# Kernel tuning notes

Measured on AMD Instinct MI355X. Metric: run time of the kernel, lower is better.

## Reference

```python
import jax, jax.numpy as jnp
import numpy as np

B, NC, NT = 1, 128, 256
F = 8                       # fidnet filters (both 1h and 13c)
KH, KW = 5, 8               # fidnet kernel
DILS = [1, 2, 3, 4, 6, 8, 10, 12, 14, 16, 18, 20, 24, 28, 32]
BLOCKS = 3
L = BLOCKS * len(DILS)      # 45 wave layers per FIDNetLayer
RSTEPS, RK = 4, 9           # refine steps / refine kernel


def dfh_tanh(x):
    return jnp.tanh(x) * 0.98 + x * 0.02


def dfh_sigmoid(x):
    return jax.nn.sigmoid(x) * 0.98 + x * 0.02


def dfh_relu(x):
    return jax.nn.relu(x) * 0.98 + x * 0.02


def conv2d(x, w, b, dil_w=1, padding='VALID'):
    # x: NHWC, w: HWIO
    out = jax.lax.conv_general_dilated(x, w, (1, 1), padding,
                                       rhs_dilation=(1, dil_w),
                                       dimension_numbers=('NHWC', 'HWIO', 'NHWC'))
    return out + b


def hilbert(x):
    # analytic signal along last axis (real input, even length)
    N = x.shape[-1]
    hh = jnp.concatenate([jnp.ones(1, jnp.float32), 2.0 * jnp.ones(N // 2 - 1, jnp.float32),
                          jnp.ones(1, jnp.float32), jnp.zeros(N // 2 - 1, jnp.float32)]).astype(jnp.complex64)
    return jnp.fft.ifft(jnp.fft.fft(x.astype(jnp.complex64)) * hh)


def fidnet_layer(x, dw, db, wy1, by1, wy2, by2, wz0, bz0):
    # WaveNet-style stack of gated dilated convs with residuals + skip sum
    x = dfh_tanh(x @ dw + db)            # (B,H,W,2F)
    skip = jnp.zeros_like(x)
    ph = (KH - 1) // 2
    for i in range(wy1.shape[0]):
        dil = DILS[i % len(DILS)]
        xin = jnp.pad(x, ((0, 0), (ph, ph), (0, dil * (KW - 1)), (0, 0)))
        y1 = dfh_tanh(conv2d(xin, wy1[i], by1[i], dil))
        y2 = dfh_sigmoid(conv2d(xin, wy2[i], by2[i], dil))
        z = jnp.pad(y1 * y2, ((0, 0), (ph, ph), (0, KW - 1), (0, 0)))
        z = conv2d(z, wz0[i], bz0[i], 1)
        skip = skip + z
        x = z + x
    return dfh_tanh(skip)


def setup_inputs():
    key = jax.random.key(0)
    ks = jax.random.split(key, 16)
    n = lambda k, s, sc=0.05: jax.random.normal(k, s, jnp.float32) * sc
    return {
        'times': n(ks[0], (B, 2, NT), 1.0),
        'times_in': n(ks[1], (B, NC), 1.0),
        'inp_2d_nc': n(ks[2], (B, 1, NC, NT), 1.0),
        'inp_2d_c': n(ks[3], (B, 1, NC, NT), 1.0),
        'c_dense_w': n(ks[4], (4, 2 * F)), 'c_dense_b': jnp.zeros((2 * F,), jnp.float32),
        'c_wy1': n(ks[5], (L, KH, KW, 2 * F, F)), 'c_by1': jnp.zeros((L, F), jnp.float32),
        'c_wy2': n(ks[6], (L, KH, KW, 2 * F, F)), 'c_by2': jnp.zeros((L, F), jnp.float32),
        'c_wz0': n(ks[7], (L, KH, KW, F, 2 * F)), 'c_bz0': jnp.zeros((L, 2 * F), jnp.float32),
        'h_dense_w': n(ks[8], (2 * F, 2 * F)), 'h_dense_b': jnp.zeros((2 * F,), jnp.float32),
        'h_wy1': n(ks[9], (L, KH, KW, 2 * F, F)), 'h_by1': jnp.zeros((L, F), jnp.float32),
        'h_wy2': n(ks[10], (L, KH, KW, 2 * F, F)), 'h_by2': jnp.zeros((L, F), jnp.float32),
        'h_wz0': n(ks[11], (L, KH, KW, F, 2 * F)), 'h_bz0': jnp.zeros((L, 2 * F), jnp.float32),
        'ref_wr': n(ks[12], (RSTEPS, RK, RK, 8 * F, 4 * F), 0.02), 'ref_br': jnp.zeros((RSTEPS, 4 * F), jnp.float32),
        'ref_wt': n(ks[13], (RSTEPS, RK, RK, 8 * F, 4 * F), 0.02), 'ref_bt': jnp.zeros((RSTEPS, 4 * F), jnp.float32),
        'dense_w': n(ks[14], (12 * F, 2)), 'dense_b': jnp.zeros((2,), jnp.float32),
    }


def reference(times, times_in, inp_2d_nc, inp_2d_c,
              c_dense_w, c_dense_b, c_wy1, c_by1, c_wy2, c_by2, c_wz0, c_bz0,
              h_dense_w, h_dense_b, h_wy1, h_by1, h_wy2, h_by2, h_wz0, h_bz0,
              ref_wr, ref_br, ref_wt, ref_bt, dense_w, dense_b):
    Bn, _, nc, nt = inp_2d_nc.shape
    # build 4-channel input plane (B, NT, NC, 4)
    times_plane = jnp.tile(times[:, :1, :], (1, nc, 1))[:, None]          # (B,1,NC,NT)
    times_in_plane = jnp.tile(times_in[:, :, None], (1, 1, nt))[:, None]  # (B,1,NC,NT)
    tr = lambda a: jnp.transpose(a, (0, 3, 2, 1))
    inp = jnp.concatenate([tr(inp_2d_nc), tr(inp_2d_c), tr(times_plane), tr(times_in_plane)], axis=-1)

    cout = fidnet_layer(inp, c_dense_w, c_dense_b, c_wy1, c_by1, c_wy2, c_by2, c_wz0, c_bz0)  # (B,NT,NC,2F)
    cout = jnp.transpose(cout, (0, 3, 1, 2))               # (B,2F,NT,NC)
    cout = jnp.pad(cout, ((0, 0), (0, 0), (0, 0), (0, nc)))  # (B,2F,NT,2NC)
    mult = jnp.concatenate([jnp.full((1,), 0.5, jnp.float32), jnp.ones(nc - 1, jnp.float32)])
    multc = mult.astype(jnp.complex64)
    cout_ft = jnp.fft.fftshift(jnp.fft.fft(multc * (cout[..., 0::2] + 1j * cout[..., 1::2])), axes=-1)
    cout_ft = jnp.transpose(jnp.real(cout_ft), (0, 1, 3, 2))  # (B,2F,NC,NT)
    cout_ft = hilbert(cout_ft)
    hinp = jnp.conj(jnp.fft.fft(jnp.fft.fftshift(cout_ft, axes=-1)) / nt)
    mult_pad = jnp.pad(mult, (0, nt - nc), constant_values=1.0).astype(jnp.complex64)
    hinp = hinp / mult_pad
    zero_mask = jnp.where(jnp.abs(times[:, 0, 2::2]) > 0.0, 1.0, 0.0)
    zero_mask = jnp.pad(zero_mask, ((0, 0), (1, 0)), constant_values=1.0)[:, None, None, :]  # (B,1,1,NT//2)
    hinp = hinp[..., :nt // 2] * zero_mask
    hinp = jnp.stack([jnp.real(hinp), jnp.imag(hinp)], axis=-1).reshape(Bn, 2 * F, nc, nt)
    hinp = jnp.transpose(hinp, (0, 2, 3, 1)).astype(jnp.float32)  # (B,NC,NT,2F)

    hout = fidnet_layer(hinp, h_dense_w, h_dense_b, h_wy1, h_by1, h_wy2, h_by2, h_wz0, h_bz0)
    hout = jnp.concatenate([hout, hinp], axis=-1)          # (B,NC,NT,4F)
    hout = jnp.transpose(hout, (0, 3, 1, 2))               # (B,4F,NC,NT)
    hout = jnp.pad(hout, ((0, 0), (0, 0), (0, 0), (0, nt)))
    winH = jnp.concatenate([jnp.full((1,), 0.5, jnp.float32), jnp.ones(nt - 1, jnp.float32)]).astype(jnp.complex64)
    hout_ft = jnp.fft.fftshift(jnp.fft.fft(winH * (hout[..., 0::2] + 1j * hout[..., 1::2])), axes=-1)
    hout_ft = jnp.transpose(jnp.real(hout_ft), (0, 2, 3, 1))  # (B,NC,NT,4F)

    fnorm = jnp.max(jnp.abs(hout_ft), axis=(1, 2, 3), keepdims=True)
    ref = jnp.tile(hout_ft / fnorm, (1, 1, 1, 2))          # (B,NC,NT,8F)
    for i in range(ref_wr.shape[0]):
        rr = dfh_relu(conv2d(ref, ref_wr[i], ref_br[i], 1, 'SAME'))
        tt = dfh_tanh(conv2d(ref, ref_wt[i], ref_bt[i], 1, 'SAME'))
        ref = jnp.concatenate([tt, rr], axis=-1) + ref
    ref = ref * fnorm
    hfin = jnp.concatenate([ref, hout_ft], axis=-1) @ dense_w + dense_b  # (B,NC,NT,2)
    return jnp.stack([hfin[..., 0], hfin[..., 1] / fnorm[..., 0]], axis=-1)
```

## Files before the change

### kernel.cpp

```cpp
#include <hip/hip_runtime.h>

#define NTT 256
#define NCC 128

typedef __attribute__((ext_vector_type(8))) short bf16x8;
typedef __attribute__((ext_vector_type(4))) float f32x4;

__device__ __forceinline__ float dfh_tanh_f(float v){ return tanhf(v)*0.98f + 0.02f*v; }
__device__ __forceinline__ float dfh_sig_f(float v){ return 0.98f/(1.f+expf(-v)) + 0.02f*v; }
__device__ __forceinline__ unsigned f2bf(float x){
  unsigned u = __float_as_uint(x);
  return (u + 0x7fffu + ((u>>16)&1u)) >> 16;
}

__global__ __launch_bounds__(256) void k_build_c(
    const float* __restrict__ times, const float* __restrict__ times_in,
    const float* __restrict__ i2nc, const float* __restrict__ i2c,
    const float* __restrict__ dw, const float* __restrict__ db,
    float* __restrict__ x, unsigned short* __restrict__ xb,
    float* __restrict__ skip)
{
  int gid = blockIdx.x*256 + threadIdx.x;
  if (gid >= NTT*NCC) return;
  int c = gid & 127, t = gid >> 7;
  float v0 = i2nc[c*NTT + t];
  float v1 = i2c [c*NTT + t];
  float v2 = times[t];
  float v3 = times_in[c];
  #pragma unroll
  for (int f=0; f<16; ++f){
    float a = v0*dw[f] + v1*dw[16+f] + v2*dw[32+f] + v3*dw[48+f] + db[f];
    float xv = dfh_tanh_f(a);
    x[gid*16+f]    = xv;
    xb[gid*16+f]   = (unsigned short)f2bf(xv);
    skip[gid*16+f] = 0.f;
  }
}

__global__ __launch_bounds__(256) void k_build_h(
    const float* __restrict__ hinp, const float* __restrict__ dw,
    const float* __restrict__ db, float* __restrict__ x,
    unsigned short* __restrict__ xb, float* __restrict__ skip)
{
  int gid = blockIdx.x*256 + threadIdx.x;
  if (gid >= NCC*NTT) return;
  const float* in = hinp + gid*16;
  float iv[16];
  #pragma unroll
  for (int i=0;i<16;i++) iv[i]=in[i];
  #pragma unroll
  for (int f=0; f<16; ++f){
    float a = db[f];
    #pragma unroll
    for (int i=0;i<16;i++) a += iv[i]*dw[i*16+f];
    float xv = dfh_tanh_f(a);
    x[gid*16+f]    = xv;
    xb[gid*16+f]   = (unsigned short)f2bf(xv);
    skip[gid*16+f] = 0.f;
  }
}

__global__ __launch_bounds__(256) void k_wpack(
    const float* __restrict__ cwy1, const float* __restrict__ cwy2,
    const float* __restrict__ cwz0,
    const float* __restrict__ hwy1, const float* __restrict__ hwy2,
    const float* __restrict__ hwz0,
    unsigned short* __restrict__ gfrag, unsigned short* __restrict__ zfrag)
{
  int tid = blockIdx.x*256 + threadIdx.x;
  if (tid < 115200){
    int lane = tid & 63, ks = (tid>>6) % 20, layer = tid / 1280;
    const float* w1 = (layer < 45) ? cwy1 + layer*5120 : hwy1 + (layer-45)*5120;
    const float* w2 = (layer < 45) ? cwy2 + layer*5120 : hwy2 + (layer-45)*5120;
    int n = lane & 15;
    unsigned pk[4];
    #pragma unroll
    for (int jj=0; jj<4; ++jj){
      unsigned hl[2];
      #pragma unroll
      for (int h2=0; h2<2; ++h2){
        int k = ks*32 + (lane>>4)*8 + jj*2 + h2;
        int tap = k>>4, ci = k&15;
        float v = (n<8) ? w1[(tap*16+ci)*8 + n] : w2[(tap*16+ci)*8 + (n-8)];
        hl[h2] = f2bf(v);
      }
      pk[jj] = hl[0] | (hl[1]<<16);
    }
    uint4 v4; v4.x=pk[0]; v4.y=pk[1]; v4.z=pk[2]; v4.w=pk[3];
    *reinterpret_cast<uint4*>(gfrag + (size_t)tid*8) = v4;
  } else if (tid < 172800){
    int t2 = tid - 115200;
    int lane = t2 & 63, ks = (t2>>6) % 10, layer = t2 / 640;
    const float* wz = (layer < 45) ? cwz0 + layer*5120 : hwz0 + (layer-45)*5120;
    int n = lane & 15;
    unsigned pk[4];
    #pragma unroll
    for (int jj=0; jj<4; ++jj){
      unsigned hl[2];
      #pragma unroll
      for (int h2=0; h2<2; ++h2){
        int k = ks*32 + (lane>>4)*8 + jj*2 + h2;
        int tap = k>>3, ci = k&7;
        hl[h2] = f2bf(wz[(tap*8+ci)*16 + n]);
      }
      pk[jj] = hl[0] | (hl[1]<<16);
    }
    uint4 v4; v4.x=pk[0]; v4.y=pk[1]; v4.z=pk[2]; v4.w=pk[3];
    *reinterpret_cast<uint4*>(zfrag + (size_t)t2*8) = v4;
  }
}

template<int W>
__global__ __launch_bounds__(512) void k_gate_mfma(
    const unsigned short* __restrict__ xb, unsigned short* __restrict__ gb,
    const unsigned short* __restrict__ bfrag,
    const float* __restrict__ by1, const float* __restrict__ by2,
    int H, int dil)
{
  __shared__ __align__(16) unsigned short lds[(10*W+1)*8];
  const int tid = threadIdx.x, lane = tid & 63, wv = tid >> 6;
  const int nb = W/128;
  const int bid = blockIdx.x;
  const int wg = (bid & 7) * (gridDim.x >> 3) + (bid >> 3);
  const int h  = wg / nb;
  const int w0 = (wg % nb) * 128;
  const int NE = 10*W;

  bf16x8 bfr[20];
  #pragma unroll
  for (int ks = 0; ks < 20; ++ks)
    bfr[ks] = *reinterpret_cast<const bf16x8*>(bfrag + (ks*64 + lane)*8);

  for (int q = tid; q < NE; q += 512){
    int q2 = q >> 1, chunk = q & 1;
    int col = q2 % W, r = q2 / W;
    int hh = h + r - 2;
    uint4 v = make_uint4(0u,0u,0u,0u);
    if (hh >= 0 && hh < H)
      v = *reinterpret_cast<const uint4*>(xb + ((size_t)(hh*W+col))*16 + chunk*8);
    *reinterpret_cast<uint4*>(lds + ((r*2+chunk)*W + col)*8) = v;
  }
  if (tid == 0) *reinterpret_cast<uint4*>(lds + (size_t)NE*8) = make_uint4(0u,0u,0u,0u);
  __syncthreads();

  f32x4 acc0 = (f32x4){0.f,0.f,0.f,0.f};
  f32x4 acc1 = (f32x4){0.f,0.f,0.f,0.f};
  const int wbase = w0 + wv*16;
  const int zoff = NE*8;
  #pragma unroll
  for (int ks = 0; ks < 20; ++ks){
    int kh = ks >> 2, kw0 = (ks & 3)*2;
    if (w0 + dil*kw0 >= W) continue;
    int kw = kw0 + (lane>>5);
    int chunk = (lane>>4) & 1;
    int col = wbase + (lane&15) + dil*kw;
    int off = (col < W) ? ((kh*2+chunk)*W + col)*8 : zoff;
    bf16x8 a = *reinterpret_cast<const bf16x8*>(lds + off);
    if (ks & 1) acc1 = __builtin_amdgcn_mfma_f32_16x16x32_bf16(a, bfr[ks], acc1, 0,0,0);
    else        acc0 = __builtin_amdgcn_mfma_f32_16x16x32_bf16(a, bfr[ks], acc0, 0,0,0);
  }

  int n = lane & 15;
  float b1 = by1[n & 7], b2 = by2[n & 7];
  #pragma unroll
  for (int ri=0; ri<4; ++ri){
    float av = acc0[ri] + acc1[ri];
    float own = av + b1;
    float oth = __shfl_xor(av, 8) + b2;
    if (n < 8){
      float gv = dfh_tanh_f(own) * dfh_sig_f(oth);
      int w = wbase + (lane>>4)*4 + ri;
      gb[((size_t)(h*W + w))*8 + n] = (unsigned short)f2bf(gv);
    }
  }
}

template<int W>
__global__ __launch_bounds__(512) void k_zres_mfma(
    const unsigned short* __restrict__ gb,
    float* __restrict__ x, unsigned short* __restrict__ xb,
    float* __restrict__ skip,
    const unsigned short* __restrict__ bfrag,
    const float* __restrict__ bz, int H)
{
  __shared__ __align__(16) unsigned short lds[(5*W+1)*8];
  const int tid = threadIdx.x, lane = tid & 63, wv = tid >> 6;
  const int nb = W/128;
  const int bid = blockIdx.x;
  const int wg = (bid & 7) * (gridDim.x >> 3) + (bid >> 3);
  const int h  = wg / nb;
  const int w0 = (wg % nb) * 128;

  bf16x8 bfr[10];
  #pragma unroll
  for (int ks = 0; ks < 10; ++ks)
    bfr[ks] = *reinterpret_cast<const bf16x8*>(bfrag + (ks*64 + lane)*8);

  for (int q = tid; q < 5*W; q += 512){
    int col = q % W, r = q / W;
    int hh = h + r - 2;
    uint4 v = make_uint4(0u,0u,0u,0u);
    if (hh >= 0 && hh < H)
      v = *reinterpret_cast<const uint4*>(gb + ((size_t)(hh*W+col))*8);
    *reinterpret_cast<uint4*>(lds + (r*W+col)*8) = v;
  }
  if (tid == 0) *reinterpret_cast<uint4*>(lds + (size_t)(5*W)*8) = make_uint4(0u,0u,0u,0u);
  __syncthreads();

  f32x4 acc0 = (f32x4){0.f,0.f,0.f,0.f};
  f32x4 acc1 = (f32x4){0.f,0.f,0.f,0.f};
  const int wbase = w0 + wv*16;
  const int zoff = 5*W*8;
  #pragma unroll
  for (int ks = 0; ks < 10; ++ks){
    int kh = ks >> 1, kw = (ks & 1)*4 + (lane>>4);
    int col = wbase + (lane&15) + kw;
    int off = (col < W) ? (kh*W + col)*8 : zoff;
    bf16x8 a = *reinterpret_cast<const bf16x8*>(lds + off);
    if (ks & 1) acc1 = __builtin_amdgcn_mfma_f32_16x16x32_bf16(a, bfr[ks], acc1, 0,0,0);
    else        acc0 = __builtin_amdgcn_mfma_f32_16x16x32_bf16(a, bfr[ks], acc0, 0,0,0);
  }

  int n = lane & 15;
  float bv = bz[n];
  #pragma unroll
  for (int ri=0; ri<4; ++ri){
    int w = wbase + (lane>>4)*4 + ri;
    size_t idx = ((size_t)(h*W + w))*16 + n;
    float z = acc0[ri] + acc1[ri] + bv;
    skip[idx] += z;
    float xn = x[idx] + z;
    x[idx]  = xn;
    xb[idx] = (unsigned short)f2bf(xn);
  }
}

__global__ __launch_bounds__(256) void k_dtanh_t(const float* __restrict__ s,
                                                 float* __restrict__ o)
{
  __shared__ float tile[256][17];
  int c = blockIdx.x;
  int tid = threadIdx.x;
  int f = tid & 15, tq = tid >> 4;
  #pragma unroll
  for (int p = 0; p < 16; ++p){
    int t = p*16 + tq;
    tile[t][f] = s[((size_t)t*128 + c)*16 + f];
  }
  __syncthreads();
  int t = tid;
  #pragma unroll
  for (int f2 = 0; f2 < 16; ++f2)
    o[(size_t)f2*32768 + c*256 + t] = dfh_tanh_f(tile[t][f2]);
}

__global__ __launch_bounds__(256) void k_dft_c1(const float* __restrict__ cout,
                                                float* __restrict__ cft)
{
  __shared__ float ctab[128], stab[128];
  int tid = threadIdx.x;
  if (tid < 128){
    float ang = (float)tid * (6.283185307179586f/128.f);
    ctab[tid] = cosf(ang); stab[tid] = sinf(ang);
  }
  __syncthreads();
  int gid = blockIdx.x*256 + tid;
  int t = gid & 255, c = (gid>>8)&127, f = gid>>15;
  int j = (c + 64) & 127;
  const float* base = cout + (size_t)f*32768 + t;
  float acc = 0.5f*base[0];
  for (int k=1; k<64; ++k){
    float re = base[(2*k)*256], im = base[(2*k+1)*256];
    int m = (j*k) & 127;
    acc += re*ctab[m] + im*stab[m];
  }
  cft[(f*128 + c)*256 + t] = acc;
}

__global__ __launch_bounds__(256) void k_dft_c2(const float* __restrict__ cft,
                                                const float* __restrict__ times,
                                                float* __restrict__ hinp)
{
  __shared__ float ctab[256], stab[256];
  int tid = threadIdx.x;
  {
    float ang = (float)tid * (6.283185307179586f/256.f);
    ctab[tid] = cosf(ang); stab[tid] = sinf(ang);
  }
  __syncthreads();
  int gid = blockIdx.x*256 + tid;
  int k = gid & 127, c = (gid>>7)&127, f = gid>>14;
  const float* r = cft + (f*128 + c)*256;
  float ar = 0.f, as = 0.f;
  for (int t=0; t<256; ++t){
    float rv = r[t];
    int m = (k*t) & 255;
    ar += rv*ctab[m];
    as += rv*stab[m];
  }
  float q;
  if (k == 0) q = 1.f/128.f;
  else {
    float mk = (fabsf(times[2*k]) > 0.f) ? 1.f : 0.f;
    q = ((k & 1) ? -1.f : 1.f) * (1.f/128.f) * mk;
  }
  float* o = hinp + (c*256 + 2*k)*16 + f;
  o[0]  = q*ar;
  o[16] = q*as;
}

__global__ __launch_bounds__(256) void k_houtcat(const float* __restrict__ skip,
                                                 const float* __restrict__ hinp,
                                                 float* __restrict__ hc,
                                                 unsigned* __restrict__ fb)
{
  int gid = blockIdx.x*256 + threadIdx.x;
  if (gid == 0) *fb = 0u;
  if (gid >= NCC*NTT) return;
  #pragma unroll
  for (int f=0; f<16; ++f){
    hc[gid*32 + f]      = dfh_tanh_f(skip[gid*16+f]);
    hc[gid*32 + 16 + f] = hinp[gid*16+f];
  }
}

__global__ __launch_bounds__(256) void k_dft_e(const float* __restrict__ hc,
                                               float* __restrict__ hft)
{
  __shared__ float ctab[256], stab[256];
  int tid = threadIdx.x;
  {
    float ang = (float)tid * (6.283185307179586f/256.f);
    ctab[tid] = cosf(ang); stab[tid] = sinf(ang);
  }
  __syncthreads();
  int gid = blockIdx.x*256 + tid;
  int f = gid & 31, t = (gid>>5)&255, c = gid>>13;
  int j = (t + 128) & 255;
  const float* base = hc + c*(256*32) + f;
  float acc = 0.5f*base[0];
  for (int k=1; k<128; ++k){
    float re = base[(2*k)*32], im = base[(2*k+1)*32];
    int m = (j*k) & 255;
    acc += re*ctab[m] + im*stab[m];
  }
  hft[(c*256 + t)*32 + f] = acc;
}

__global__ __launch_bounds__(256) void k_fnorm(const float* __restrict__ hft,
                                               unsigned* __restrict__ fb, int n)
{
  __shared__ float red[4];
  float m = 0.f;
  const float4* p = reinterpret_cast<const float4*>(hft);
  int n4 = n >> 2;
  for (int i = blockIdx.x*256 + threadIdx.x; i < n4; i += gridDim.x*256){
    float4 v = p[i];
    m = fmaxf(m, fmaxf(fmaxf(fabsf(v.x), fabsf(v.y)),
                       fmaxf(fabsf(v.z), fabsf(v.w))));
  }
  #pragma unroll
  for (int off=32; off>0; off>>=1) m = fmaxf(m, __shfl_down(m, off));
  if ((threadIdx.x & 63) == 0) red[threadIdx.x >> 6] = m;
  __syncthreads();
  if (threadIdx.x == 0){
    float mm = fmaxf(fmaxf(red[0], red[1]), fmaxf(red[2], red[3]));
    atomicMax(fb, __float_as_uint(mm));
  }
}

__global__ __launch_bounds__(256) void k_refinit(const float* __restrict__ hft,
                                                 const unsigned* __restrict__ fb,
                                                 float* __restrict__ ref)
{
  int gid = blockIdx.x*256 + threadIdx.x;
  if (gid >= NCC*NTT*64) return;
  float fn = __uint_as_float(*fb);
  int f = gid & 63, ct = gid >> 6;
  ref[gid] = hft[ct*32 + (f & 31)] / fn;
}

__global__ __launch_bounds__(256) void k_wconv4(
    const float* __restrict__ wt0, const float* __restrict__ wr0,
    unsigned short* __restrict__ bfrag)
{
  int gid = blockIdx.x*256 + threadIdx.x;
  if (gid >= 4*648*64) return;
  int step = gid / 41472, rem = gid % 41472;
  int lane = rem & 63, frag = rem >> 6;
  int nt = frag & 3, kt = (frag>>2) & 1, p = frag >> 3;
  const float* wt = wt0 + step*165888;
  const float* wr = wr0 + step*165888;
  int o = nt*16 + (lane & 15);
  int ci0 = kt*32 + (lane>>4)*8;
  const float* src = (o < 32) ? (wt + (p*64 + ci0)*32 + o)
                              : (wr + (p*64 + ci0)*32 + (o-32));
  unsigned pk[4];
  #pragma unroll
  for (int j=0;j<4;++j)
    pk[j] = f2bf(src[(2*j)*32]) | (f2bf(src[(2*j+1)*32]) << 16);
  uint4 v; v.x = pk[0]; v.y = pk[1]; v.z = pk[2]; v.w = pk[3];
  *reinterpret_cast<uint4*>(bfrag + (size_t)gid*8) = v;
}

__device__ __forceinline__ void ref_stage_load2(const float* __restrict__ srcf,
    int c, int kh, int t0, int tid, float4 (&fr)[2][2])
{
  int cc = c + kh - 4;
  #pragma unroll
  for (int r2=0; r2<2; ++r2){
    float4 z = make_float4(0.f,0.f,0.f,0.f);
    fr[r2][0] = z; fr[r2][1] = z;
    int q = tid + r2*256;
    if (q < 320){
      int row = q >> 3, c16 = q & 7;
      int t = t0 - 4 + row;
      if (t >= 0 && t < 256){
        const float* sp = srcf + ((size_t)(cc*256 + t))*64 + c16*8;
        fr[r2][0] = *reinterpret_cast<const float4*>(sp);
        fr[r2][1] = *reinterpret_cast<const float4*>(sp + 4);
      }
    }
  }
}

__device__ __forceinline__ void ref_stage_write2(unsigned short* lds,
    int tid, float4 (&fr)[2][2])
{
  #pragma unroll
  for (int r2=0; r2<2; ++r2){
    int q = tid + r2*256;
    if (q < 320){
      int row = q >> 3, c16 = q & 7;
      uint4 v;
      v.x = f2bf(fr[r2][0].x) | (f2bf(fr[r2][0].y)<<16);
      v.y = f2bf(fr[r2][0].z) | (f2bf(fr[r2][0].w)<<16);
      v.z = f2bf(fr[r2][1].x) | (f2bf(fr[r2][1].y)<<16);
      v.w = f2bf(fr[r2][1].z) | (f2bf(fr[r2][1].w)<<16);
      *reinterpret_cast<uint4*>(&lds[row*64 + ((c16 ^ (row&7))*8)]) = v;
    }
  }
}

__global__ __launch_bounds__(256) void k_refmfma(
    const float* __restrict__ srcf, float* __restrict__ dstf,
    const unsigned short* __restrict__ bfrag,
    const float* __restrict__ bt, const float* __restrict__ br)
{
  __shared__ __align__(16) unsigned short ldsA[2][40*64];
  __shared__ float redbuf[2][16][65];
  const int tid = threadIdx.x, lane = tid & 63, wv = tid >> 6;
  const int mt = wv & 1, kt = wv >> 1;
  int bid = blockIdx.x;
  int wg = (bid & 7)*128 + (bid >> 3);
  const int c  = wg >> 3;
  const int t0 = (wg & 7) * 32;

  f32x4 acc[4];
  #pragma unroll
  for (int nt=0; nt<4; ++nt) acc[nt] = (f32x4){0.f,0.f,0.f,0.f};

  const int kh0 = (c < 4)   ? 4 - c   : 0;
  const int kh1 = (c > 123) ? 131 - c : 8;

  float4 fr[2][2];
  ref_stage_load2(srcf, c, kh0, t0, tid, fr);
  int cur = 0;
  for (int kh = kh0; kh <= kh1; ++kh){
    ref_stage_write2(ldsA[cur], tid, fr);
    __syncthreads();
    if (kh < kh1) ref_stage_load2(srcf, c, kh+1, t0, tid, fr);
    for (int kw=0; kw<9; ++kw){
      const int p = kh*9 + kw;
      const unsigned short* bb = bfrag + (size_t)p*4096;
      bf16x8 b[4];
      #pragma unroll
      for (int nt=0; nt<4; ++nt)
        b[nt] = *reinterpret_cast<const bf16x8*>(bb + ((kt*4+nt)*64 + lane)*8);
      const int j = mt*16 + (lane&15) + kw;
      bf16x8 a = *reinterpret_cast<const bf16x8*>(
          &ldsA[cur][j*64 + (((kt*4 + (lane>>4)) ^ (j&7))*8)]);
      #pragma unroll
      for (int nt=0; nt<4; ++nt)
        acc[nt] = __builtin_amdgcn_mfma_f32_16x16x32_bf16(a, b[nt], acc[nt], 0,0,0);
    }
    __syncthreads();
    cur ^= 1;
  }

  if (kt == 1){
    #pragma unroll
    for (int nt=0; nt<4; ++nt)
      #pragma unroll
      for (int ri=0; ri<4; ++ri)
        redbuf[mt][nt*4+ri][lane] = acc[nt][ri];
  }
  __syncthreads();
  if (kt == 0){
    #pragma unroll
    for (int nt=0; nt<4; ++nt){
      int o = nt*16 + (lane&15);
      float bv = (o < 32) ? bt[o] : br[o-32];
      #pragma unroll
      for (int ri=0; ri<4; ++ri){
        int t = t0 + mt*16 + (lane>>4)*4 + ri;
        float v = acc[nt][ri] + redbuf[mt][nt*4+ri][lane] + bv;
        v = (nt < 2) ? dfh_tanh_f(v) : (v > 0.f ? v : 0.02f*v);
        size_t idx = ((size_t)(c*256 + t))*64 + o;
        dstf[idx] = v + srcf[idx];
      }
    }
  }
}

__global__ __launch_bounds__(256) void k_final(const float* __restrict__ ref,
                                               const float* __restrict__ hft,
                                               const unsigned* __restrict__ fb,
                                               const float* __restrict__ dw,
                                               const float* __restrict__ db,
                                               float* __restrict__ out)
{
  int gid = blockIdx.x*256 + threadIdx.x;
  if (gid >= NCC*NTT) return;
  float fn = __uint_as_float(*fb);
  const float* rp = ref + gid*64;
  const float* hp = hft + gid*32;
  float s0 = db[0], s1 = db[1];
  #pragma unroll 8
  for (int f=0; f<64; ++f){ float v = rp[f]*fn; s0 += v*dw[f*2]; s1 += v*dw[f*2+1]; }
  #pragma unroll 8
  for (int f=0; f<32; ++f){ float v = hp[f]; s0 += v*dw[(64+f)*2]; s1 += v*dw[(64+f)*2+1]; }
  out[gid*2]   = s0;
  out[gid*2+1] = s1/fn;
}

extern "C" void kernel_launch(void* const* d_in, const int* in_sizes, int n_in,
                              void* d_out, int out_size, void* d_ws, size_t ws_size,
                              hipStream_t stream)
{
  const float* times    = (const float*)d_in[0];
  const float* times_in = (const float*)d_in[1];
  const float* i2nc     = (const float*)d_in[2];
  const float* i2c      = (const float*)d_in[3];
  const float* cdw  = (const float*)d_in[4];  const float* cdb  = (const float*)d_in[5];
  const float* cwy1 = (const float*)d_in[6];  const float* cby1 = (const float*)d_in[7];
  const float* cwy2 = (const float*)d_in[8];  const float* cby2 = (const float*)d_in[9];
  const float* cwz0 = (const float*)d_in[10]; const float* cbz0 = (const float*)d_in[11];
  const float* hdw  = (const float*)d_in[12]; const float* hdb  = (const float*)d_in[13];
  const float* hwy1 = (const float*)d_in[14]; const float* hby1 = (const float*)d_in[15];
  const float* hwy2 = (const float*)d_in[16]; const float* hby2 = (const float*)d_in[17];
  const float* hwz0 = (const float*)d_in[18]; const float* hbz0 = (const float*)d_in[19];
  const float* rwr  = (const float*)d_in[20]; const float* rbr  = (const float*)d_in[21];
  const float* rwt  = (const float*)d_in[22]; const float* rbt  = (const float*)d_in[23];
  const float* fdw  = (const float*)d_in[24]; const float* fdb  = (const float*)d_in[25];
  float* out = (float*)d_out;

  float* ws = (float*)d_ws;
  float* A   = ws;
  float* Bb  = ws + 524288;
  float* C   = ws + 1048576;
  unsigned short* xb = (unsigned short*)(ws + 1572864);
  unsigned short* gb = (unsigned short*)(ws + 1835008);
  float* hcat = ws + 1966080;
  float* hft  = ws + 3014656;
  unsigned short* gfrag  = (unsigned short*)(ws + 4146176);
  unsigned short* zfrag  = (unsigned short*)(ws + 4606976);
  float* refA = ws;
  unsigned short* bfrag4 = (unsigned short*)(ws + 2097152);
  float* refB = ws + 4146176;
  unsigned* fb = (unsigned*)(ws + 6243328);

  float* x_c = A;  float* skp_c = Bb; float* cout = C;
  float* cft = A;  float* hinp  = Bb; float* x_h  = C; float* skp_h = A;

  static const int DILS[15] = {1,2,3,4,6,8,10,12,14,16,18,20,24,28,32};

  k_wpack<<<675,256,0,stream>>>(cwy1, cwy2, cwz0, hwy1, hwy2, hwz0, gfrag, zfrag);

  k_build_c<<<128,256,0,stream>>>(times, times_in, i2nc, i2c, cdw, cdb, x_c, xb, skp_c);
  for (int i=0; i<45; ++i){
    int dil = DILS[i % 15];
    k_gate_mfma<128><<<256,512,0,stream>>>(xb, gb, gfrag + (size_t)i*10240,
                                           cby1 + i*8, cby2 + i*8, 256, dil);
    k_zres_mfma<128><<<256,512,0,stream>>>(gb, x_c, xb, skp_c, zfrag + (size_t)i*5120,
                                           cbz0 + i*16, 256);
  }
  k_dtanh_t<<<128,256,0,stream>>>(skp_c, cout);

  k_dft_c1<<<2048,256,0,stream>>>(cout, cft);
  k_dft_c2<<<1024,256,0,stream>>>(cft, times, hinp);

  k_build_h<<<128,256,0,stream>>>(hinp, hdw, hdb, x_h, xb, skp_h);
  for (int i=0; i<45; ++i){
    int dil = DILS[i % 15];
    k_gate_mfma<256><<<256,512,0,stream>>>(xb, gb, gfrag + (size_t)(45+i)*10240,
                                           hby1 + i*8, hby2 + i*8, 128, dil);
    k_zres_mfma<256><<<256,512,0,stream>>>(gb, x_h, xb, skp_h, zfrag + (size_t)(45+i)*5120,
                                           hbz0 + i*16, 128);
  }
  k_houtcat<<<128,256,0,stream>>>(skp_h, hinp, hcat, fb);

  k_dft_e<<<4096,256,0,stream>>>(hcat, hft);
  k_fnorm<<<256,256,0,stream>>>(hft, fb, 1048576);

  k_wconv4<<<648,256,0,stream>>>(rwt, rwr, bfrag4);
  k_refinit<<<8192,256,0,stream>>>(hft, fb, refA);
  float* rsrc = refA; float* rdst = refB;
  for (int i=0; i<4; ++i){
    k_refmfma<<<1024,256,0,stream>>>(rsrc, rdst, bfrag4 + (size_t)i*331776,
                                     rbt + i*32, rbr + i*32);
    float* tmp = rsrc; rsrc = rdst; rdst = tmp;
  }

  k_final<<<128,256,0,stream>>>(rsrc, hft, fb, fdw, fdb, out);
}
```

Baseline: 1.244 ms.

## Preload all nine refine-conv input rows into LDS before the MFMA loop

The refine conv kernel used to double-buffer one kernel-row slab at a time, with two barriers per kh step. It now stages all nine input rows, zero-filled at the borders, into a larger LDS buffer up front with a single barrier, then runs a barrier-free MFMA loop with the kw loop unrolled. The intent is to remove the per-row synchronisation and shorten the dependency chain between loads and compute. In exchange, LDS use grows to about 46 KB per block, which can lower occupancy, and the load phase no longer overlaps with compute. Boundary channels now always run all nine kh steps on zeros instead of skipping them.

```diff
diff --git a/kernel.cpp b/kernel.cpp
--- a/kernel.cpp
+++ b/kernel.cpp
@@ -403,51 +403,12 @@
   *reinterpret_cast<uint4*>(bfrag + (size_t)gid*8) = v;
 }
 
-__device__ __forceinline__ void ref_stage_load2(const float* __restrict__ srcf,
-    int c, int kh, int t0, int tid, float4 (&fr)[2][2])
-{
-  int cc = c + kh - 4;
-  #pragma unroll
-  for (int r2=0; r2<2; ++r2){
-    float4 z = make_float4(0.f,0.f,0.f,0.f);
-    fr[r2][0] = z; fr[r2][1] = z;
-    int q = tid + r2*256;
-    if (q < 320){
-      int row = q >> 3, c16 = q & 7;
-      int t = t0 - 4 + row;
-      if (t >= 0 && t < 256){
-        const float* sp = srcf + ((size_t)(cc*256 + t))*64 + c16*8;
-        fr[r2][0] = *reinterpret_cast<const float4*>(sp);
-        fr[r2][1] = *reinterpret_cast<const float4*>(sp + 4);
-      }
-    }
-  }
-}
-
-__device__ __forceinline__ void ref_stage_write2(unsigned short* lds,
-    int tid, float4 (&fr)[2][2])
-{
-  #pragma unroll
-  for (int r2=0; r2<2; ++r2){
-    int q = tid + r2*256;
-    if (q < 320){
-      int row = q >> 3, c16 = q & 7;
-      uint4 v;
-      v.x = f2bf(fr[r2][0].x) | (f2bf(fr[r2][0].y)<<16);
-      v.y = f2bf(fr[r2][0].z) | (f2bf(fr[r2][0].w)<<16);
-      v.z = f2bf(fr[r2][1].x) | (f2bf(fr[r2][1].y)<<16);
-      v.w = f2bf(fr[r2][1].z) | (f2bf(fr[r2][1].w)<<16);
-      *reinterpret_cast<uint4*>(&lds[row*64 + ((c16 ^ (row&7))*8)]) = v;
-    }
-  }
-}
-
 __global__ __launch_bounds__(256) void k_refmfma(
     const float* __restrict__ srcf, float* __restrict__ dstf,
     const unsigned short* __restrict__ bfrag,
     const float* __restrict__ bt, const float* __restrict__ br)
 {
-  __shared__ __align__(16) unsigned short ldsA[2][40*64];
+  __shared__ __align__(16) unsigned short ldsA[9*40*64];
   __shared__ float redbuf[2][16][65];
   const int tid = threadIdx.x, lane = tid & 63, wv = tid >> 6;
   const int mt = wv & 1, kt = wv >> 1;
@@ -456,20 +417,31 @@
   const int c  = wg >> 3;
   const int t0 = (wg & 7) * 32;
 
+  for (int q = tid; q < 9*320; q += 256){
+    int r9 = q / 320, rem = q % 320;
+    int row = rem >> 3, c16 = rem & 7;
+    int cc = c + r9 - 4;
+    int t  = t0 - 4 + row;
+    uint4 v = make_uint4(0u,0u,0u,0u);
+    if (cc >= 0 && cc < 128 && t >= 0 && t < 256){
+      const float* sp = srcf + ((size_t)(cc*256 + t))*64 + c16*8;
+      float4 f0 = *reinterpret_cast<const float4*>(sp);
+      float4 f1 = *reinterpret_cast<const float4*>(sp + 4);
+      v.x = f2bf(f0.x) | (f2bf(f0.y)<<16);
+      v.y = f2bf(f0.z) | (f2bf(f0.w)<<16);
+      v.z = f2bf(f1.x) | (f2bf(f1.y)<<16);
+      v.w = f2bf(f1.z) | (f2bf(f1.w)<<16);
+    }
+    *reinterpret_cast<uint4*>(&ldsA[r9*2560 + row*64 + ((c16 ^ (row&7))*8)]) = v;
+  }
+  __syncthreads();
+
   f32x4 acc[4];
   #pragma unroll
   for (int nt=0; nt<4; ++nt) acc[nt] = (f32x4){0.f,0.f,0.f,0.f};
 
-  const int kh0 = (c < 4)   ? 4 - c   : 0;
-  const int kh1 = (c > 123) ? 131 - c : 8;
-
-  float4 fr[2][2];
-  ref_stage_load2(srcf, c, kh0, t0, tid, fr);
-  int cur = 0;
-  for (int kh = kh0; kh <= kh1; ++kh){
-    ref_stage_write2(ldsA[cur], tid, fr);
-    __syncthreads();
-    if (kh < kh1) ref_stage_load2(srcf, c, kh+1, t0, tid, fr);
+  for (int kh = 0; kh < 9; ++kh){
+    #pragma unroll
     for (int kw=0; kw<9; ++kw){
       const int p = kh*9 + kw;
       const unsigned short* bb = bfrag + (size_t)p*4096;
@@ -479,13 +451,11 @@
         b[nt] = *reinterpret_cast<const bf16x8*>(bb + ((kt*4+nt)*64 + lane)*8);
       const int j = mt*16 + (lane&15) + kw;
       bf16x8 a = *reinterpret_cast<const bf16x8*>(
-          &ldsA[cur][j*64 + (((kt*4 + (lane>>4)) ^ (j&7))*8)]);
+          &ldsA[kh*2560 + j*64 + (((kt*4 + (lane>>4)) ^ (j&7))*8)]);
       #pragma unroll
       for (int nt=0; nt<4; ++nt)
         acc[nt] = __builtin_amdgcn_mfma_f32_16x16x32_bf16(a, b[nt], acc[nt], 0,0,0);
     }
-    __syncthreads();
-    cur ^= 1;
   }
 
   if (kt == 1){
```

Measured after the change: 1.253 ms. No clear change (+0.6%).
